# Kernel optimization log

Hardware: AMD Instinct MI355X
Metric: run time of the kernel (lower is better)

Reference implementation:

```python
import jax, jax.numpy as jnp
import numpy as np

N, E, G = 50000, 800000, 512
DIN, HID, DOUT, L, DE = 64, 64, 128, 3, 16
NEG_SLOPE = 0.2
BN_EPS = 1e-5


def setup_inputs() -> dict:
    key = jax.random.key(0)
    ks = jax.random.split(key, 20)
    s = 0.1  # weight scale for numerical stability
    return {
        "x": jax.random.normal(ks[0], (N, DIN), jnp.float32),
        "edge_index": jax.random.randint(ks[1], (2, E), 0, N, jnp.int32),
        "edge_attr": jax.random.normal(ks[2], (E, DE), jnp.float32),
        "batch": jnp.sort(jax.random.randint(ks[3], (N,), 0, G, jnp.int32)),
        "emb_W": jax.random.normal(ks[4], (HID, DIN), jnp.float32) * s,
        "emb_b": jax.random.normal(ks[5], (HID,), jnp.float32) * s,
        "Wl": jax.random.normal(ks[6], (L, HID, HID), jnp.float32) * s,
        "bl": jax.random.normal(ks[7], (L, HID), jnp.float32) * s,
        "Wr": jax.random.normal(ks[8], (L, HID, HID), jnp.float32) * s,
        "br": jax.random.normal(ks[9], (L, HID), jnp.float32) * s,
        "We": jax.random.normal(ks[10], (L, HID, DE), jnp.float32) * s,
        "att": jax.random.normal(ks[11], (L, HID), jnp.float32) * s,
        "conv_bias": jax.random.normal(ks[12], (L, HID), jnp.float32) * s,
        "bn_gamma": jax.random.uniform(ks[13], (L, HID), jnp.float32, 0.5, 1.5),
        "bn_beta": jax.random.normal(ks[14], (L, HID), jnp.float32) * s,
        "bn_mean": jnp.zeros((L, HID), jnp.float32),
        "bn_var": jnp.ones((L, HID), jnp.float32),
        "lin_W": jax.random.normal(ks[15], (DOUT, HID), jnp.float32) * s,
        "lin_b": jax.random.normal(ks[16], (DOUT,), jnp.float32) * s,
    }


def _gatv2(h, src, dst, edge_attr, Wl, bl, Wr, br, We, att, bias):
    # GATv2Conv, heads=1, concat=False, with edge features
    xl = h @ Wl.T + bl                      # [N,C] source transform (also message value)
    xr = h @ Wr.T + br                      # [N,C] target transform
    ea = edge_attr @ We.T                   # [E,C]
    m = xl[src] + xr[dst] + ea              # [E,C]
    m = jax.nn.leaky_relu(m, NEG_SLOPE)
    alpha = m @ att                         # [E] attention logits
    amax = jax.ops.segment_max(alpha, dst, num_segments=N)
    ea_exp = jnp.exp(alpha - amax[dst])
    denom = jax.ops.segment_sum(ea_exp, dst, num_segments=N)
    alpha = ea_exp / (denom[dst] + 1e-16)
    out = jax.ops.segment_sum(alpha[:, None] * xl[src], dst, num_segments=N)
    return out + bias


def reference(x, edge_index, edge_attr, batch, emb_W, emb_b, Wl, bl, Wr, br,
              We, att, conv_bias, bn_gamma, bn_beta, bn_mean, bn_var, lin_W, lin_b):
    src, dst = edge_index[0], edge_index[1]
    h = x @ emb_W.T + emb_b
    for i in range(L):
        hc = _gatv2(h, src, dst, edge_attr, Wl[i], bl[i], Wr[i], br[i],
                    We[i], att[i], conv_bias[i])
        # BatchNorm (eval mode, running stats)
        hc = (hc - bn_mean[i]) * jax.lax.rsqrt(bn_var[i] + BN_EPS) * bn_gamma[i] + bn_beta[i]
        hc = jax.nn.gelu(hc, approximate=False)  # torch F.gelu default is exact erf
        h = h + hc                                # residual; dropout p=0 / eval -> identity
    out = h @ lin_W.T + lin_b                     # [N,DOUT]
    counts = jax.ops.segment_sum(jnp.ones((N,), out.dtype), batch, num_segments=G)
    pooled = jax.ops.segment_sum(out, batch, num_segments=G)
    return pooled / jnp.maximum(counts, 1.0)[:, None]
```

## Files before the change

kernel.cpp:

```cpp
#include <hip/hip_runtime.h>
#include <math.h>

#define NEG_SLOPE 0.2f
#define BN_EPS 1e-5f

template <int N> struct IC { static constexpr int v = N; };
template <bool B> struct BC { static constexpr bool v = B; };

typedef _Float16 half2v __attribute__((ext_vector_type(2)));
typedef _Float16 f16x8 __attribute__((ext_vector_type(8)));
typedef float f32x4v __attribute__((ext_vector_type(4)));

__device__ __forceinline__ half2v u2h(unsigned u) {
  union { unsigned u; half2v h; } c;
  c.u = u;
  return c.h;
}
__device__ __forceinline__ unsigned pkh(float lo, float hi) {
  union { half2v h; unsigned u; } c;
  c.h[0] = (_Float16)lo;
  c.h[1] = (_Float16)hi;
  return c.u;
}

#if defined(__has_builtin)
#if __has_builtin(__builtin_amdgcn_fdot2)
#define FDOT2(a, b, c) __builtin_amdgcn_fdot2((a), (b), (c), false)
#endif
#endif
#ifndef FDOT2
__device__ __forceinline__ float fdot2_sw(half2v a, half2v b, float c) {
  return c + (float)a[0] * (float)b[0] + (float)a[1] * (float)b[1];
}
#define FDOT2(a, b, c) fdot2_sw((a), (b), (c))
#endif

#if defined(__has_builtin)
#if __has_builtin(__builtin_amdgcn_exp2f)
#define FEXP(x) __builtin_amdgcn_exp2f(x)
#define ATT_SCALE 1.44269504088896f
#endif
#endif
#ifndef FEXP
#define FEXP(x) __expf(x)
#define ATT_SCALE 1.0f
#endif

#define FMA4(acc, v, wq) \
  acc += (v).x * (wq).x + (v).y * (wq).y + (v).z * (wq).z + (v).w * (wq).w

#define DOT_ROW(buf, stride, r, bias, OUT)                                  \
  {                                                                         \
    __builtin_amdgcn_sched_barrier(0);                                      \
    float a0 = 0.f, a1 = 0.f, a2 = 0.f, a3 = 0.f;                           \
    _Pragma("unroll") for (int q = 0; q < 4; q++) {                         \
      float4 v0 = *(const float4*)((buf) + (r) * (stride) + q * 16 + 0);    \
      float4 v1 = *(const float4*)((buf) + (r) * (stride) + q * 16 + 4);    \
      float4 v2 = *(const float4*)((buf) + (r) * (stride) + q * 16 + 8);    \
      float4 v3 = *(const float4*)((buf) + (r) * (stride) + q * 16 + 12);   \
      FMA4(a0, v0, W[q * 4 + 0]);                                           \
      FMA4(a1, v1, W[q * 4 + 1]);                                           \
      FMA4(a2, v2, W[q * 4 + 2]);                                           \
      FMA4(a3, v3, W[q * 4 + 3]);                                           \
    }                                                                       \
    OUT = (bias) + ((a0 + a1) + (a2 + a3));                                 \
  }

__device__ __forceinline__ float wave_sum64(float v) {
  int x;
  x = __builtin_amdgcn_update_dpp(0, __float_as_int(v), 0x121, 0xF, 0xF, true);
  v += __int_as_float(x);
  x = __builtin_amdgcn_update_dpp(0, __float_as_int(v), 0x122, 0xF, 0xF, true);
  v += __int_as_float(x);
  x = __builtin_amdgcn_update_dpp(0, __float_as_int(v), 0x124, 0xF, 0xF, true);
  v += __int_as_float(x);
  x = __builtin_amdgcn_update_dpp(0, __float_as_int(v), 0x128, 0xF, 0xF, true);
  v += __int_as_float(x);
  x = __builtin_amdgcn_update_dpp(0, __float_as_int(v), 0x142, 0xF, 0xF, true);
  v += __int_as_float(x);
  x = __builtin_amdgcn_update_dpp(0, __float_as_int(v), 0x143, 0xF, 0xF, true);
  v += __int_as_float(x);
  return __int_as_float(__builtin_amdgcn_readlane(__float_as_int(v), 63));
}

#if defined(__has_builtin)
#if __has_builtin(__builtin_amdgcn_mfma_f32_16x16x32_f16)
#define HAVE_MFMA16 1
#endif
#endif

__global__ __launch_bounds__(256) void hist_kernel(
    const int* __restrict__ dst, const int* __restrict__ batch,
    int* __restrict__ deg, float* __restrict__ counts,
    const float* __restrict__ Wl, const float* __restrict__ Wr,
    _Float16* __restrict__ w16, int E_, int N_) {
  int i = blockIdx.x * 256 + threadIdx.x;
  if (i < E_) atomicAdd(&deg[dst[i]], 1);
  if (i < N_) atomicAdd(&counts[batch[i]], 1.0f);
  if (i < 24576)
    w16[i] = (i < 12288) ? (_Float16)Wl[i] : (_Float16)Wr[i - 12288];
}

__global__ __launch_bounds__(256) void scanA_kernel(
    const int* __restrict__ deg, int* __restrict__ row_ptr,
    int* __restrict__ segTot, int* __restrict__ bins, int N_, int nseg) {
  __shared__ int sb[256];
  __shared__ int lb[128];
  int t = threadIdx.x;
  if (t < 128) lb[t] = 0;
  __syncthreads();
  for (int s = blockIdx.x; s < nseg; s += gridDim.x) {
    int i = s * 256 + t;
    int v = (i < N_) ? deg[i] : 0;
    if (i < N_) atomicAdd(&lb[127 - min(v, 127)], 1);
    sb[t] = v;
    __syncthreads();
    for (int off = 1; off < 256; off <<= 1) {
      int a = (t >= off) ? sb[t - off] : 0;
      __syncthreads();
      sb[t] += a;
      __syncthreads();
    }
    int incl = sb[t];
    if (i < N_) row_ptr[i] = incl - v;
    if (t == 255) segTot[s] = incl;
    __syncthreads();
  }
  if (t < 128 && lb[t]) atomicAdd(&bins[t], lb[t]);
}

__global__ __launch_bounds__(256) void scanB_kernel(int* __restrict__ segTot,
                                                    int* __restrict__ bins,
                                                    int nseg) {
  __shared__ int sb[256];
  __shared__ int baseSh;
  int t = threadIdx.x;
  if (t == 0) baseSh = 0;
  __syncthreads();
  for (int c0 = 0; c0 < nseg; c0 += 256) {
    int s = c0 + t;
    int v = (s < nseg) ? segTot[s] : 0;
    sb[t] = v;
    __syncthreads();
    for (int off = 1; off < 256; off <<= 1) {
      int a = (t >= off) ? sb[t - off] : 0;
      __syncthreads();
      sb[t] += a;
      __syncthreads();
    }
    int incl = sb[t];
    int base = baseSh;
    if (s < nseg) segTot[s] = base + incl - v;
    __syncthreads();
    if (t == 255) baseSh = base + incl;
    __syncthreads();
  }
  int v2 = (t < 128) ? bins[t] : 0;
  sb[t] = v2;
  __syncthreads();
  for (int off = 1; off < 256; off <<= 1) {
    int a = (t >= off) ? sb[t - off] : 0;
    __syncthreads();
    sb[t] += a;
    __syncthreads();
  }
  if (t < 128) bins[t] = sb[t] - v2;
}

__global__ __launch_bounds__(256) void scanC_kernel(
    int* __restrict__ row_ptr, const int* __restrict__ segTot,
    int* __restrict__ cursor, const int* __restrict__ deg,
    int* __restrict__ bins, int* __restrict__ perm,
    int* __restrict__ csr_src, int* __restrict__ csr_eid, int N_, int E_) {
  __shared__ int lb[128];
  __shared__ int lbase[128];
  int t = threadIdx.x;
  if (t < 128) lb[t] = 0;
  __syncthreads();
  int i = blockIdx.x * 256 + t;
  int bin = 0, rk = 0;
  bool ok = (i < N_);
  if (ok) {
    int rp = row_ptr[i] + segTot[i >> 8];
    row_ptr[i] = rp;
    cursor[i] = rp;
    int dg = deg[i];
    bin = 127 - min(dg, 127);
    rk = atomicAdd(&lb[bin], 1);
  }
  if (i == 0) row_ptr[N_] = E_;
  if (blockIdx.x == 0 && t < 16) {
    csr_src[E_ + t] = 0;
    csr_eid[E_ + t] = 0;
  }
  __syncthreads();
  if (t < 128) {
    int c = lb[t];
    lbase[t] = c ? atomicAdd(&bins[t], c) : 0;
  }
  __syncthreads();
  if (ok) perm[lbase[bin] + rk] = i;
}

__global__ __launch_bounds__(256) void scatter_kernel(
    const int* __restrict__ src, const int* __restrict__ dst,
    int* __restrict__ cursor, int* __restrict__ csr_src,
    int* __restrict__ csr_eid, int E_) {
  int e = blockIdx.x * 256 + threadIdx.x;
  if (e >= E_) return;
  int pos = atomicAdd(&cursor[dst[e]], 1);
  csr_src[pos] = src[e];
  csr_eid[pos] = e;
}

__global__ __launch_bounds__(256) void permute_attr_kernel(
    const float4* __restrict__ edge_attr4, const int* __restrict__ csr_eid,
    unsigned* __restrict__ attr_u, int E_) {
  int p = blockIdx.x * 256 + threadIdx.x;
  if (p >= E_) return;
  int e = csr_eid[p];
  float4 a0 = edge_attr4[(size_t)e * 4 + 0];
  float4 a1 = edge_attr4[(size_t)e * 4 + 1];
  float4 a2 = edge_attr4[(size_t)e * 4 + 2];
  float4 a3 = edge_attr4[(size_t)e * 4 + 3];
  uint4 u0, u1;
  u0.x = pkh(a0.x, a0.y);
  u0.y = pkh(a0.z, a0.w);
  u0.z = pkh(a1.x, a1.y);
  u0.w = pkh(a1.z, a1.w);
  u1.x = pkh(a2.x, a2.y);
  u1.y = pkh(a2.z, a2.w);
  u1.z = pkh(a3.x, a3.y);
  u1.w = pkh(a3.z, a3.w);
  uint4* d4 = (uint4*)(attr_u + (size_t)p * 8);
  d4[0] = u0;
  d4[1] = u1;
}

__global__ __launch_bounds__(256, 3) void emb_kernel(
    const float* __restrict__ x, const float* __restrict__ emb_W,
    const float* __restrict__ emb_b, const _Float16* __restrict__ Wl16,
    const float* __restrict__ bl, const _Float16* __restrict__ Wr16,
    const float* __restrict__ br, float* __restrict__ h,
    _Float16* __restrict__ xl, _Float16* __restrict__ xr, int rows) {
  __shared__ float sx[4096];
  __shared__ float sh[64 * 68];
  int lane = threadIdx.x & 63;
  int w = threadIdx.x >> 6;
  int n0 = blockIdx.x * 64;

  {
    int gmax = rows * 64 - 4;
#pragma unroll
    for (int i = 0; i < 4; i++) {
      int off = w * 1024 + i * 256 + lane * 4;
      int g = min(n0 * 64 + off, gmax);
      *(float4*)(sx + off) = *(const float4*)(x + g);
    }
  }

  {
    float4 W[16];
#pragma unroll
    for (int q = 0; q < 16; q++) W[q] = ((const float4*)(emb_W + lane * 64))[q];
    float b = emb_b[lane];
#pragma unroll 1
    for (int t = 0; t < 16; t++) {
      int r = w * 16 + t;
      float a;
      DOT_ROW(sx, 64, r, b, a);
      sh[r * 68 + lane] = a;
      int n = n0 + r;
      if (n < rows) h[(size_t)n * 64 + lane] = a;
    }
  }

#ifdef HAVE_MFMA16
  {
    int r = lane & 15;
    int kg = lane >> 4;
    int nb = n0 + w * 16;
    const float* p = sh + (w * 16 + r) * 68 + kg * 8;
    f16x8 A0, A1;
    {
      float4 xa = *(const float4*)(p);
      float4 xb = *(const float4*)(p + 4);
      A0[0] = (_Float16)xa.x; A0[1] = (_Float16)xa.y;
      A0[2] = (_Float16)xa.z; A0[3] = (_Float16)xa.w;
      A0[4] = (_Float16)xb.x; A0[5] = (_Float16)xb.y;
      A0[6] = (_Float16)xb.z; A0[7] = (_Float16)xb.w;
      xa = *(const float4*)(p + 32);
      xb = *(const float4*)(p + 36);
      A1[0] = (_Float16)xa.x; A1[1] = (_Float16)xa.y;
      A1[2] = (_Float16)xa.z; A1[3] = (_Float16)xa.w;
      A1[4] = (_Float16)xb.x; A1[5] = (_Float16)xb.y;
      A1[6] = (_Float16)xb.z; A1[7] = (_Float16)xb.w;
    }
#pragma unroll
    for (int c = 0; c < 4; c++) {
      int o = c * 16 + r;
      {
        const f16x8* b0 = (const f16x8*)(Wl16 + (size_t)o * 64 + kg * 8);
        const f16x8* b1 = (const f16x8*)(Wl16 + (size_t)o * 64 + 32 + kg * 8);
        f32x4v acc;
        float bv = bl[o];
        acc[0] = bv; acc[1] = bv; acc[2] = bv; acc[3] = bv;
        acc = __builtin_amdgcn_mfma_f32_16x16x32_f16(A0, b0[0], acc, 0, 0, 0);
        acc = __builtin_amdgcn_mfma_f32_16x16x32_f16(A1, b1[0], acc, 0, 0, 0);
#pragma unroll
        for (int g = 0; g < 4; g++) {
          int nd = nb + kg * 4 + g;
          if (nd < rows) xl[(size_t)nd * 64 + o] = (_Float16)acc[g];
        }
      }
      {
        const f16x8* b0 = (const f16x8*)(Wr16 + (size_t)o * 64 + kg * 8);
        const f16x8* b1 = (const f16x8*)(Wr16 + (size_t)o * 64 + 32 + kg * 8);
        f32x4v acc;
        float bv = br[o];
        acc[0] = bv; acc[1] = bv; acc[2] = bv; acc[3] = bv;
        acc = __builtin_amdgcn_mfma_f32_16x16x32_f16(A0, b0[0], acc, 0, 0, 0);
        acc = __builtin_amdgcn_mfma_f32_16x16x32_f16(A1, b1[0], acc, 0, 0, 0);
#pragma unroll
        for (int g = 0; g < 4; g++) {
          int nd = nb + kg * 4 + g;
          if (nd < rows) xr[(size_t)nd * 64 + o] = (_Float16)acc[g];
        }
      }
    }
  }
#endif
}

__global__ __launch_bounds__(256) void linx_mfma_kernel(
    const float* __restrict__ in, const _Float16* __restrict__ Wl16,
    const float* __restrict__ bl, const _Float16* __restrict__ Wr16,
    const float* __restrict__ br, _Float16* __restrict__ xl,
    _Float16* __restrict__ xr, int rows) {
#ifdef HAVE_MFMA16
  int lane = threadIdx.x & 63;
  int w = threadIdx.x >> 6;
  int n0 = blockIdx.x * 64 + w * 16;
  int r = lane & 15;
  int kg = lane >> 4;

  int nA = min(n0 + r, rows - 1);
  f16x8 A0, A1;
  {
    const float* p = in + (size_t)nA * 64 + kg * 8;
    float4 xa = *(const float4*)(p);
    float4 xb = *(const float4*)(p + 4);
    A0[0] = (_Float16)xa.x; A0[1] = (_Float16)xa.y;
    A0[2] = (_Float16)xa.z; A0[3] = (_Float16)xa.w;
    A0[4] = (_Float16)xb.x; A0[5] = (_Float16)xb.y;
    A0[6] = (_Float16)xb.z; A0[7] = (_Float16)xb.w;
    xa = *(const float4*)(p + 32);
    xb = *(const float4*)(p + 36);
    A1[0] = (_Float16)xa.x; A1[1] = (_Float16)xa.y;
    A1[2] = (_Float16)xa.z; A1[3] = (_Float16)xa.w;
    A1[4] = (_Float16)xb.x; A1[5] = (_Float16)xb.y;
    A1[6] = (_Float16)xb.z; A1[7] = (_Float16)xb.w;
  }

#pragma unroll
  for (int c = 0; c < 4; c++) {
    int o = c * 16 + r;
    {
      const f16x8* b0 = (const f16x8*)(Wl16 + (size_t)o * 64 + kg * 8);
      const f16x8* b1 = (const f16x8*)(Wl16 + (size_t)o * 64 + 32 + kg * 8);
      f32x4v acc;
      float bv = bl[o];
      acc[0] = bv; acc[1] = bv; acc[2] = bv; acc[3] = bv;
      acc = __builtin_amdgcn_mfma_f32_16x16x32_f16(A0, b0[0], acc, 0, 0, 0);
      acc = __builtin_amdgcn_mfma_f32_16x16x32_f16(A1, b1[0], acc, 0, 0, 0);
#pragma unroll
      for (int g = 0; g < 4; g++) {
        int nd = n0 + kg * 4 + g;
        if (nd < rows) xl[(size_t)nd * 64 + o] = (_Float16)acc[g];
      }
    }
    {
      const f16x8* b0 = (const f16x8*)(Wr16 + (size_t)o * 64 + kg * 8);
      const f16x8* b1 = (const f16x8*)(Wr16 + (size_t)o * 64 + 32 + kg * 8);
      f32x4v acc;
      float bv = br[o];
      acc[0] = bv; acc[1] = bv; acc[2] = bv; acc[3] = bv;
      acc = __builtin_amdgcn_mfma_f32_16x16x32_f16(A0, b0[0], acc, 0, 0, 0);
      acc = __builtin_amdgcn_mfma_f32_16x16x32_f16(A1, b1[0], acc, 0, 0, 0);
#pragma unroll
      for (int g = 0; g < 4; g++) {
        int nd = n0 + kg * 4 + g;
        if (nd < rows) xr[(size_t)nd * 64 + o] = (_Float16)acc[g];
      }
    }
  }
#endif
}

template <bool CONTIG>
__global__ __launch_bounds__(256) void gat_fused_kernel(
    const int* __restrict__ perm, const int* __restrict__ csr_src,
    const int* __restrict__ csr_eid, const int* __restrict__ row_ptr,
    const unsigned* __restrict__ attr_u, const float* __restrict__ edge_attr,
    const _Float16* __restrict__ xl, const _Float16* __restrict__ xr,
    const float* __restrict__ We, const float* __restrict__ att,
    const float* __restrict__ conv_bias, const float* __restrict__ gamma,
    const float* __restrict__ beta, const float* __restrict__ mean,
    const float* __restrict__ var, float* __restrict__ h, int N_) {
  int widx = (blockIdx.x * 256 + threadIdx.x) >> 6;
  if (widx >= N_) return;
  int d = __builtin_amdgcn_readfirstlane(perm[widx]);
  int j = threadIdx.x & 63;
  half2v Wek2[8];
  float Wekf[16];
  if constexpr (CONTIG) {
#pragma unroll
    for (int q = 0; q < 8; q++) {
      Wek2[q][0] = (_Float16)We[j * 16 + 2 * q];
      Wek2[q][1] = (_Float16)We[j * 16 + 2 * q + 1];
    }
  } else {
#pragma unroll
    for (int k = 0; k < 16; k++) Wekf[k] = We[j * 16 + k];
  }
  float att_j = att[j] * ATT_SCALE;
  float sc = rsqrtf(var[j] + BN_EPS) * gamma[j];
  float sh = (conv_bias[j] - mean[j]) * sc + beta[j];

  int beg = __builtin_amdgcn_readfirstlane(row_ptr[d]);
  int end = __builtin_amdgcn_readfirstlane(row_ptr[d + 1]);
  float xrj = (float)xr[(size_t)d * 64 + j];
  float m = -INFINITY, l = 0.f, acc = 0.f;

  auto chunk = [&](int base, auto C_, auto PAD_) {
    constexpr int C = decltype(C_)::v;
    constexpr bool PAD = decltype(PAD_)::v;
    int si[C];
#pragma unroll
    for (int t = 0; t < C; t++) {
      int idx = PAD ? min(base + t, end - 1) : (base + t);
      si[t] = __builtin_amdgcn_readfirstlane(csr_src[idx]);
    }
    float xlv[C];
#pragma unroll
    for (int t = 0; t < C; t++)
      xlv[t] = (float)xl[(size_t)si[t] * 64 + j];
    float v[C];
#pragma unroll
    for (int t = 0; t < C; t++) {
      int idx = PAD ? min(base + t, end - 1) : (base + t);
      float ea;
      if constexpr (CONTIG) {
        const uint4* ap = (const uint4*)(attr_u + (size_t)idx * 8);
        uint4 ua = ap[0], ub = ap[1];
        ea = 0.f;
        ea = FDOT2(u2h(ua.x), Wek2[0], ea);
        ea = FDOT2(u2h(ua.y), Wek2[1], ea);
        ea = FDOT2(u2h(ua.z), Wek2[2], ea);
        ea = FDOT2(u2h(ua.w), Wek2[3], ea);
        ea = FDOT2(u2h(ub.x), Wek2[4], ea);
        ea = FDOT2(u2h(ub.y), Wek2[5], ea);
        ea = FDOT2(u2h(ub.z), Wek2[6], ea);
        ea = FDOT2(u2h(ub.w), Wek2[7], ea);
      } else {
        const float4* ap =
            (const float4*)(edge_attr + (size_t)csr_eid[idx] * 16);
        float4 a0 = ap[0], a1 = ap[1], a2 = ap[2], a3 = ap[3];
        ea = a0.x * Wekf[0]  + a0.y * Wekf[1]  + a0.z * Wekf[2]  + a0.w * Wekf[3]
           + a1.x * Wekf[4]  + a1.y * Wekf[5]  + a1.z * Wekf[6]  + a1.w * Wekf[7]
           + a2.x * Wekf[8]  + a2.y * Wekf[9]  + a2.z * Wekf[10] + a2.w * Wekf[11]
           + a3.x * Wekf[12] + a3.y * Wekf[13] + a3.z * Wekf[14] + a3.w * Wekf[15];
      }
      float z = xlv[t] + xrj + ea;
      z = fmaxf(z, NEG_SLOPE * z);
      float p = wave_sum64(z * att_j);
      v[t] = (!PAD || (base + t < end)) ? p : -INFINITY;
    }
    float mc = v[0];
#pragma unroll
    for (int t = 1; t < C; t++) mc = fmaxf(mc, v[t]);
    float newm = fmaxf(m, mc);
    float s = FEXP(m - newm);
    l *= s;
    acc *= s;
#pragma unroll
    for (int t = 0; t < C; t++) {
      float w = FEXP(v[t] - newm);
      l += w;
      acc += w * xlv[t];
    }
    m = newm;
  };

  int base = beg;
  for (; base + 16 <= end; base += 16) chunk(base, IC<16>{}, BC<false>{});
  if (base + 8 <= end) {
    chunk(base, IC<8>{}, BC<false>{});
    base += 8;
  }
  if (base + 4 <= end) {
    chunk(base, IC<4>{}, BC<false>{});
    base += 4;
  }
  if (base < end) chunk(base, IC<4>{}, BC<true>{});

  float val = acc / (l + 1e-16f) * sc + sh;
  float g = 0.5f * val * (1.f + erff(val * 0.70710678118654752f));
  h[(size_t)d * 64 + j] += g;
}

__global__ __launch_bounds__(256, 2) void lin_pool_kernel(
    const float* __restrict__ h, const float* __restrict__ lin_W,
    const float* __restrict__ lin_b, const int* __restrict__ batch,
    const float* __restrict__ counts, float* __restrict__ pooled, int rows) {
  __shared__ float shh[4096];
  int lane = threadIdx.x & 63;
  int w = threadIdx.x >> 6;
  int n0 = blockIdx.x * 64;

  {
    int gmax = rows * 64 - 4;
#pragma unroll
    for (int i = 0; i < 4; i++) {
      int off = w * 1024 + i * 256 + lane * 4;
      int g = min(n0 * 64 + off, gmax);
      *(float4*)(shh + off) = *(const float4*)(h + g);
    }
  }

  float4 W0[16], W1[16];
#pragma unroll
  for (int q = 0; q < 16; q++) W0[q] = ((const float4*)(lin_W + lane * 64))[q];
#pragma unroll
  for (int q = 0; q < 16; q++)
    W1[q] = ((const float4*)(lin_W + (lane + 64) * 64))[q];
  float b0 = lin_b[lane], b1 = lin_b[lane + 64];

  int curg = -1;
  float acc0 = 0.f, acc1 = 0.f;
  int lim = min(16, rows - n0 - w * 16);
#pragma unroll 1
  for (int t = 0; t < lim; t++) {
    int r = w * 16 + t;
    __builtin_amdgcn_sched_barrier(0);
    float d0 = b0, d1 = b1;
#pragma unroll
    for (int q = 0; q < 16; q++) {
      float4 v = *(const float4*)(shh + r * 64 + q * 4);
      FMA4(d0, v, W0[q]);
      FMA4(d1, v, W1[q]);
    }
    int g = batch[n0 + r];
    if (g != curg) {
      if (curg >= 0) {
        float inv = 1.f / fmaxf(counts[curg], 1.f);
        atomicAdd(&pooled[curg * 128 + lane], acc0 * inv);
        atomicAdd(&pooled[curg * 128 + 64 + lane], acc1 * inv);
      }
      curg = g;
      acc0 = 0.f;
      acc1 = 0.f;
    }
    acc0 += d0;
    acc1 += d1;
  }
  if (curg >= 0) {
    float inv = 1.f / fmaxf(counts[curg], 1.f);
    atomicAdd(&pooled[curg * 128 + lane], acc0 * inv);
    atomicAdd(&pooled[curg * 128 + 64 + lane], acc1 * inv);
  }
}

extern "C" void kernel_launch(void* const* d_in, const int* in_sizes, int n_in,
                              void* d_out, int out_size, void* d_ws, size_t ws_size,
                              hipStream_t stream) {
  const float* x         = (const float*)d_in[0];
  const int*   edge_index= (const int*)  d_in[1];
  const float* edge_attr = (const float*)d_in[2];
  const int*   batch     = (const int*)  d_in[3];
  const float* emb_W     = (const float*)d_in[4];
  const float* emb_b     = (const float*)d_in[5];
  const float* Wl        = (const float*)d_in[6];
  const float* bl        = (const float*)d_in[7];
  const float* Wr        = (const float*)d_in[8];
  const float* br        = (const float*)d_in[9];
  const float* We        = (const float*)d_in[10];
  const float* att       = (const float*)d_in[11];
  const float* conv_bias = (const float*)d_in[12];
  const float* bn_gamma  = (const float*)d_in[13];
  const float* bn_beta   = (const float*)d_in[14];
  const float* bn_mean   = (const float*)d_in[15];
  const float* bn_var    = (const float*)d_in[16];
  const float* lin_W     = (const float*)d_in[17];
  const float* lin_b     = (const float*)d_in[18];

  const int N_ = in_sizes[0] / 64;
  const int E_ = in_sizes[1] / 2;
  const int G_ = out_size / 128;
  const int* src = edge_index;
  const int* dst = edge_index + E_;

  const int Npad = (N_ + 3) & ~3;
  const int Epad = (E_ + 19) & ~3;
  const int nseg = (N_ + 255) / 256;

  float* ws      = (float*)d_ws;
  float* h       = ws;
  _Float16* xl   = (_Float16*)(h + (size_t)N_ * 64);
  _Float16* xr   = xl + (size_t)N_ * 64;
  int*   csr_src = (int*)(xr + (size_t)N_ * 64);
  int*   csr_eid = csr_src + Epad;
  int*   row_ptr = csr_eid + Epad;
  int*   cursor  = row_ptr + (Npad + 4);
  int*   deg     = cursor + Npad;
  float* counts  = (float*)(deg + Npad);
  int*   segTot  = (int*)(counts + G_);
  int*   bins    = segTot + nseg + 8;
  int*   perm    = bins + 128;
  uintptr_t abp  = (uintptr_t)(perm + Npad);
  abp = (abp + 15) & ~(uintptr_t)15;
  _Float16* w16  = (_Float16*)abp;
  uintptr_t abp2 = abp + 24576 * sizeof(_Float16);
  unsigned* attr_u = (unsigned*)abp2;

  size_t base_bytes = (abp2 - (uintptr_t)d_ws);
  bool contig = ws_size >= base_bytes + (size_t)E_ * 32 + 64;

  const int hgrid = (max(E_, N_) + 255) / 256;
  const int ngrid = (N_ + 255) / 256;
  const int egrid = (E_ + 255) / 256;

  hipMemsetAsync(deg, 0, ((size_t)Npad + G_ + nseg + 8 + 128) * 4, stream);
  hist_kernel<<<hgrid, 256, 0, stream>>>(dst, batch, deg, counts, Wl, Wr,
                                         w16, E_, N_);
  scanA_kernel<<<min(nseg, 1024), 256, 0, stream>>>(deg, row_ptr, segTot,
                                                    bins, N_, nseg);
  scanB_kernel<<<1, 256, 0, stream>>>(segTot, bins, nseg);
  scanC_kernel<<<ngrid, 256, 0, stream>>>(row_ptr, segTot, cursor, deg, bins,
                                          perm, csr_src, csr_eid, N_, E_);
  scatter_kernel<<<egrid, 256, 0, stream>>>(src, dst, cursor, csr_src,
                                            csr_eid, E_);
  if (contig) {
    permute_attr_kernel<<<egrid, 256, 0, stream>>>(
        (const float4*)edge_attr, csr_eid, attr_u, E_);
  }

  const int tgrid = (N_ + 63) / 64;
  emb_kernel<<<tgrid, 256, 0, stream>>>(x, emb_W, emb_b, w16, bl,
                                        w16 + 12288, br, h, xl, xr, N_);

  const int gatBlocks = (N_ + 3) / 4;
  for (int l = 0; l < 3; l++) {
    if (l > 0) {
      linx_mfma_kernel<<<tgrid, 256, 0, stream>>>(
          h, w16 + (size_t)l * 4096, bl + l * 64,
          w16 + 12288 + (size_t)l * 4096, br + l * 64, xl, xr, N_);
    }
    if (contig) {
      gat_fused_kernel<true><<<gatBlocks, 256, 0, stream>>>(
          perm, csr_src, csr_eid, row_ptr, attr_u, edge_attr, xl, xr,
          We + (size_t)l * 1024, att + l * 64, conv_bias + l * 64,
          bn_gamma + l * 64, bn_beta + l * 64, bn_mean + l * 64,
          bn_var + l * 64, h, N_);
    } else {
      gat_fused_kernel<false><<<gatBlocks, 256, 0, stream>>>(
          perm, csr_src, csr_eid, row_ptr, attr_u, edge_attr, xl, xr,
          We + (size_t)l * 1024, att + l * 64, conv_bias + l * 64,
          bn_gamma + l * 64, bn_beta + l * 64, bn_mean + l * 64,
          bn_var + l * 64, h, N_);
    }
  }

  hipMemsetAsync(d_out, 0, (size_t)G_ * 128 * 4, stream);
  lin_pool_kernel<<<(N_ + 63) / 64, 256, 0, stream>>>(
      h, lin_W, lin_b, batch, counts, (float*)d_out, N_);
}
```

Baseline: 544.8 us.

## Process four edges per wave in GAT kernel with 16 lanes per edge

Result: slower. 628.6 us (+15.4%).

```diff
diff --git a/kernel.cpp b/kernel.cpp
--- a/kernel.cpp
+++ b/kernel.cpp
@@ -5,7 +5,6 @@
 #define BN_EPS 1e-5f
 
 template <int N> struct IC { static constexpr int v = N; };
-template <bool B> struct BC { static constexpr bool v = B; };
 
 typedef _Float16 half2v __attribute__((ext_vector_type(2)));
 typedef _Float16 f16x8 __attribute__((ext_vector_type(8)));
@@ -66,7 +65,7 @@
     OUT = (bias) + ((a0 + a1) + (a2 + a3));                                 \
   }
 
-__device__ __forceinline__ float wave_sum64(float v) {
+__device__ __forceinline__ float row_sum16(float v) {
   int x;
   x = __builtin_amdgcn_update_dpp(0, __float_as_int(v), 0x121, 0xF, 0xF, true);
   v += __int_as_float(x);
@@ -76,11 +75,7 @@
   v += __int_as_float(x);
   x = __builtin_amdgcn_update_dpp(0, __float_as_int(v), 0x128, 0xF, 0xF, true);
   v += __int_as_float(x);
-  x = __builtin_amdgcn_update_dpp(0, __float_as_int(v), 0x142, 0xF, 0xF, true);
-  v += __int_as_float(x);
-  x = __builtin_amdgcn_update_dpp(0, __float_as_int(v), 0x143, 0xF, 0xF, true);
-  v += __int_as_float(x);
-  return __int_as_float(__builtin_amdgcn_readlane(__float_as_int(v), 63));
+  return v;
 }
 
 #if defined(__has_builtin)
@@ -93,12 +88,18 @@
     const int* __restrict__ dst, const int* __restrict__ batch,
     int* __restrict__ deg, float* __restrict__ counts,
     const float* __restrict__ Wl, const float* __restrict__ Wr,
-    _Float16* __restrict__ w16, int E_, int N_) {
+    const float* __restrict__ We, _Float16* __restrict__ w16, int E_,
+    int N_) {
   int i = blockIdx.x * 256 + threadIdx.x;
   if (i < E_) atomicAdd(&deg[dst[i]], 1);
   if (i < N_) atomicAdd(&counts[batch[i]], 1.0f);
-  if (i < 24576)
-    w16[i] = (i < 12288) ? (_Float16)Wl[i] : (_Float16)Wr[i - 12288];
+  if (i < 12288) {
+    w16[i] = (_Float16)Wl[i];
+  } else if (i < 24576) {
+    w16[i] = (_Float16)Wr[i - 12288];
+  } else if (i < 27648) {
+    w16[i] = (_Float16)We[i - 24576];
+  }
 }
 
 __global__ __launch_bounds__(256) void scanA_kernel(
@@ -403,110 +404,214 @@
     const int* __restrict__ csr_eid, const int* __restrict__ row_ptr,
     const unsigned* __restrict__ attr_u, const float* __restrict__ edge_attr,
     const _Float16* __restrict__ xl, const _Float16* __restrict__ xr,
-    const float* __restrict__ We, const float* __restrict__ att,
-    const float* __restrict__ conv_bias, const float* __restrict__ gamma,
-    const float* __restrict__ beta, const float* __restrict__ mean,
-    const float* __restrict__ var, float* __restrict__ h, int N_) {
+    const _Float16* __restrict__ we16, const float* __restrict__ We,
+    const float* __restrict__ att, const float* __restrict__ conv_bias,
+    const float* __restrict__ gamma, const float* __restrict__ beta,
+    const float* __restrict__ mean, const float* __restrict__ var,
+    float* __restrict__ h, int N_) {
   int widx = (blockIdx.x * 256 + threadIdx.x) >> 6;
   if (widx >= N_) return;
   int d = __builtin_amdgcn_readfirstlane(perm[widx]);
-  int j = threadIdx.x & 63;
-  half2v Wek2[8];
-  float Wekf[16];
+  int lane = threadIdx.x & 63;
+  int jj = lane & 15;
+  int eg = lane >> 4;
+
+  half2v Wk[4][8];
+  float Wf[4][16];
   if constexpr (CONTIG) {
-#pragma unroll
-    for (int q = 0; q < 8; q++) {
-      Wek2[q][0] = (_Float16)We[j * 16 + 2 * q];
-      Wek2[q][1] = (_Float16)We[j * 16 + 2 * q + 1];
+    const uint4* wp = (const uint4*)(we16 + jj * 64);
+#pragma unroll
+    for (int i = 0; i < 4; i++) {
+      uint4 wa = wp[2 * i], wb = wp[2 * i + 1];
+      Wk[i][0] = u2h(wa.x);
+      Wk[i][1] = u2h(wa.y);
+      Wk[i][2] = u2h(wa.z);
+      Wk[i][3] = u2h(wa.w);
+      Wk[i][4] = u2h(wb.x);
+      Wk[i][5] = u2h(wb.y);
+      Wk[i][6] = u2h(wb.z);
+      Wk[i][7] = u2h(wb.w);
     }
   } else {
 #pragma unroll
-    for (int k = 0; k < 16; k++) Wekf[k] = We[j * 16 + k];
-  }
-  float att_j = att[j] * ATT_SCALE;
-  float sc = rsqrtf(var[j] + BN_EPS) * gamma[j];
-  float sh = (conv_bias[j] - mean[j]) * sc + beta[j];
+    for (int i = 0; i < 4; i++)
+#pragma unroll
+      for (int k = 0; k < 16; k++) Wf[i][k] = We[(4 * jj + i) * 16 + k];
+  }
+  float4 attv = *(const float4*)(att + jj * 4);
+  float at0 = attv.x * ATT_SCALE, at1 = attv.y * ATT_SCALE;
+  float at2 = attv.z * ATT_SCALE, at3 = attv.w * ATT_SCALE;
+  float4 varv = *(const float4*)(var + jj * 4);
+  float4 gamv = *(const float4*)(gamma + jj * 4);
+  float4 cbv = *(const float4*)(conv_bias + jj * 4);
+  float4 mev = *(const float4*)(mean + jj * 4);
+  float4 bev = *(const float4*)(beta + jj * 4);
+  float sc0 = rsqrtf(varv.x + BN_EPS) * gamv.x;
+  float sh0 = (cbv.x - mev.x) * sc0 + bev.x;
+  float sc1 = rsqrtf(varv.y + BN_EPS) * gamv.y;
+  float sh1 = (cbv.y - mev.y) * sc1 + bev.y;
+  float sc2 = rsqrtf(varv.z + BN_EPS) * gamv.z;
+  float sh2 = (cbv.z - mev.z) * sc2 + bev.z;
+  float sc3 = rsqrtf(varv.w + BN_EPS) * gamv.w;
+  float sh3 = (cbv.w - mev.w) * sc3 + bev.w;
 
   int beg = __builtin_amdgcn_readfirstlane(row_ptr[d]);
   int end = __builtin_amdgcn_readfirstlane(row_ptr[d + 1]);
-  float xrj = (float)xr[(size_t)d * 64 + j];
-  float m = -INFINITY, l = 0.f, acc = 0.f;
-
-  auto chunk = [&](int base, auto C_, auto PAD_) {
+  int deg = end - beg;
+  int degm1 = max(deg - 1, 0);
+
+  float xr0, xr1, xr2, xr3;
+  {
+    uint2 xp = *(const uint2*)((const char*)xr + (size_t)d * 128 + jj * 8);
+    half2v h0 = u2h(xp.x), h1 = u2h(xp.y);
+    xr0 = (float)h0[0];
+    xr1 = (float)h0[1];
+    xr2 = (float)h1[0];
+    xr3 = (float)h1[1];
+  }
+
+  float m = -INFINITY, l = 0.f;
+  float a0 = 0.f, a1 = 0.f, a2 = 0.f, a3 = 0.f;
+
+  auto chunk = [&](int base, auto C_) {
     constexpr int C = decltype(C_)::v;
-    constexpr bool PAD = decltype(PAD_)::v;
+    int idxv[C];
+    bool msk[C];
+#pragma unroll
+    for (int k = 0; k < C; k++) {
+      int t = base + k * 4 + eg;
+      idxv[k] = beg + min(t, degm1);
+      msk[k] = t < deg;
+    }
     int si[C];
 #pragma unroll
-    for (int t = 0; t < C; t++) {
-      int idx = PAD ? min(base + t, end - 1) : (base + t);
-      si[t] = __builtin_amdgcn_readfirstlane(csr_src[idx]);
-    }
-    float xlv[C];
-#pragma unroll
-    for (int t = 0; t < C; t++)
-      xlv[t] = (float)xl[(size_t)si[t] * 64 + j];
+    for (int k = 0; k < C; k++) si[k] = csr_src[idxv[k]];
+    uint2 xpk[C];
+#pragma unroll
+    for (int k = 0; k < C; k++)
+      xpk[k] = *(const uint2*)((const char*)xl + (size_t)si[k] * 128 + jj * 8);
     float v[C];
 #pragma unroll
-    for (int t = 0; t < C; t++) {
-      int idx = PAD ? min(base + t, end - 1) : (base + t);
-      float ea;
+    for (int k = 0; k < C; k++) {
+      float ea0, ea1, ea2, ea3;
       if constexpr (CONTIG) {
-        const uint4* ap = (const uint4*)(attr_u + (size_t)idx * 8);
+        const uint4* ap = (const uint4*)(attr_u + (size_t)idxv[k] * 8);
         uint4 ua = ap[0], ub = ap[1];
-        ea = 0.f;
-        ea = FDOT2(u2h(ua.x), Wek2[0], ea);
-        ea = FDOT2(u2h(ua.y), Wek2[1], ea);
-        ea = FDOT2(u2h(ua.z), Wek2[2], ea);
-        ea = FDOT2(u2h(ua.w), Wek2[3], ea);
-        ea = FDOT2(u2h(ub.x), Wek2[4], ea);
-        ea = FDOT2(u2h(ub.y), Wek2[5], ea);
-        ea = FDOT2(u2h(ub.z), Wek2[6], ea);
-        ea = FDOT2(u2h(ub.w), Wek2[7], ea);
+        ea0 = 0.f; ea1 = 0.f; ea2 = 0.f; ea3 = 0.f;
+        half2v c0 = u2h(ua.x), c1 = u2h(ua.y), c2 = u2h(ua.z), c3 = u2h(ua.w);
+        half2v c4 = u2h(ub.x), c5 = u2h(ub.y), c6 = u2h(ub.z), c7 = u2h(ub.w);
+        ea0 = FDOT2(c0, Wk[0][0], ea0); ea0 = FDOT2(c1, Wk[0][1], ea0);
+        ea0 = FDOT2(c2, Wk[0][2], ea0); ea0 = FDOT2(c3, Wk[0][3], ea0);
+        ea0 = FDOT2(c4, Wk[0][4], ea0); ea0 = FDOT2(c5, Wk[0][5], ea0);
+        ea0 = FDOT2(c6, Wk[0][6], ea0); ea0 = FDOT2(c7, Wk[0][7], ea0);
+        ea1 = FDOT2(c0, Wk[1][0], ea1); ea1 = FDOT2(c1, Wk[1][1], ea1);
+        ea1 = FDOT2(c2, Wk[1][2], ea1); ea1 = FDOT2(c3, Wk[1][3], ea1);
+        ea1 = FDOT2(c4, Wk[1][4], ea1); ea1 = FDOT2(c5, Wk[1][5], ea1);
+        ea1 = FDOT2(c6, Wk[1][6], ea1); ea1 = FDOT2(c7, Wk[1][7], ea1);
+        ea2 = FDOT2(c0, Wk[2][0], ea2); ea2 = FDOT2(c1, Wk[2][1], ea2);
+        ea2 = FDOT2(c2, Wk[2][2], ea2); ea2 = FDOT2(c3, Wk[2][3], ea2);
+        ea2 = FDOT2(c4, Wk[2][4], ea2); ea2 = FDOT2(c5, Wk[2][5], ea2);
+        ea2 = FDOT2(c6, Wk[2][6], ea2); ea2 = FDOT2(c7, Wk[2][7], ea2);
+        ea3 = FDOT2(c0, Wk[3][0], ea3); ea3 = FDOT2(c1, Wk[3][1], ea3);
+        ea3 = FDOT2(c2, Wk[3][2], ea3); ea3 = FDOT2(c3, Wk[3][3], ea3);
+        ea3 = FDOT2(c4, Wk[3][4], ea3); ea3 = FDOT2(c5, Wk[3][5], ea3);
+        ea3 = FDOT2(c6, Wk[3][6], ea3); ea3 = FDOT2(c7, Wk[3][7], ea3);
       } else {
-        const float4* ap =
-            (const float4*)(edge_attr + (size_t)csr_eid[idx] * 16);
-        float4 a0 = ap[0], a1 = ap[1], a2 = ap[2], a3 = ap[3];
-        ea = a0.x * Wekf[0]  + a0.y * Wekf[1]  + a0.z * Wekf[2]  + a0.w * Wekf[3]
-           + a1.x * Wekf[4]  + a1.y * Wekf[5]  + a1.z * Wekf[6]  + a1.w * Wekf[7]
-           + a2.x * Wekf[8]  + a2.y * Wekf[9]  + a2.z * Wekf[10] + a2.w * Wekf[11]
-           + a3.x * Wekf[12] + a3.y * Wekf[13] + a3.z * Wekf[14] + a3.w * Wekf[15];
+        int e = csr_eid[idxv[k]];
+        const float4* ap = (const float4*)(edge_attr + (size_t)e * 16);
+        float4 q0 = ap[0], q1 = ap[1], q2 = ap[2], q3 = ap[3];
+        ea0 = q0.x * Wf[0][0] + q0.y * Wf[0][1] + q0.z * Wf[0][2] + q0.w * Wf[0][3]
+            + q1.x * Wf[0][4] + q1.y * Wf[0][5] + q1.z * Wf[0][6] + q1.w * Wf[0][7]
+            + q2.x * Wf[0][8] + q2.y * Wf[0][9] + q2.z * Wf[0][10] + q2.w * Wf[0][11]
+            + q3.x * Wf[0][12] + q3.y * Wf[0][13] + q3.z * Wf[0][14] + q3.w * Wf[0][15];
+        ea1 = q0.x * Wf[1][0] + q0.y * Wf[1][1] + q0.z * Wf[1][2] + q0.w * Wf[1][3]
+            + q1.x * Wf[1][4] + q1.y * Wf[1][5] + q1.z * Wf[1][6] + q1.w * Wf[1][7]
+            + q2.x * Wf[1][8] + q2.y * Wf[1][9] + q2.z * Wf[1][10] + q2.w * Wf[1][11]
+            + q3.x * Wf[1][12] + q3.y * Wf[1][13] + q3.z * Wf[1][14] + q3.w * Wf[1][15];
+        ea2 = q0.x * Wf[2][0] + q0.y * Wf[2][1] + q0.z * Wf[2][2] + q0.w * Wf[2][3]
+            + q1.x * Wf[2][4] + q1.y * Wf[2][5] + q1.z * Wf[2][6] + q1.w * Wf[2][7]
+            + q2.x * Wf[2][8] + q2.y * Wf[2][9] + q2.z * Wf[2][10] + q2.w * Wf[2][11]
+            + q3.x * Wf[2][12] + q3.y * Wf[2][13] + q3.z * Wf[2][14] + q3.w * Wf[2][15];
+        ea3 = q0.x * Wf[3][0] + q0.y * Wf[3][1] + q0.z * Wf[3][2] + q0.w * Wf[3][3]
+            + q1.x * Wf[3][4] + q1.y * Wf[3][5] + q1.z * Wf[3][6] + q1.w * Wf[3][7]
+            + q2.x * Wf[3][8] + q2.y * Wf[3][9] + q2.z * Wf[3][10] + q2.w * Wf[3][11]
+            + q3.x * Wf[3][12] + q3.y * Wf[3][13] + q3.z * Wf[3][14] + q3.w * Wf[3][15];
       }
-      float z = xlv[t] + xrj + ea;
-      z = fmaxf(z, NEG_SLOPE * z);
-      float p = wave_sum64(z * att_j);
-      v[t] = (!PAD || (base + t < end)) ? p : -INFINITY;
+      half2v h0 = u2h(xpk[k].x), h1 = u2h(xpk[k].y);
+      float z0 = (float)h0[0] + xr0 + ea0;
+      z0 = fmaxf(z0, NEG_SLOPE * z0);
+      float z1 = (float)h0[1] + xr1 + ea1;
+      z1 = fmaxf(z1, NEG_SLOPE * z1);
+      float z2 = (float)h1[0] + xr2 + ea2;
+      z2 = fmaxf(z2, NEG_SLOPE * z2);
+      float z3 = (float)h1[1] + xr3 + ea3;
+      z3 = fmaxf(z3, NEG_SLOPE * z3);
+      float p = (z0 * at0 + z1 * at1) + (z2 * at2 + z3 * at3);
+      p = row_sum16(p);
+      v[k] = msk[k] ? p : -INFINITY;
     }
     float mc = v[0];
 #pragma unroll
-    for (int t = 1; t < C; t++) mc = fmaxf(mc, v[t]);
+    for (int k = 1; k < C; k++) mc = fmaxf(mc, v[k]);
+    mc = fmaxf(mc, __shfl_xor(mc, 16, 64));
+    mc = fmaxf(mc, __shfl_xor(mc, 32, 64));
     float newm = fmaxf(m, mc);
     float s = FEXP(m - newm);
     l *= s;
-    acc *= s;
-#pragma unroll
-    for (int t = 0; t < C; t++) {
-      float w = FEXP(v[t] - newm);
+    a0 *= s;
+    a1 *= s;
+    a2 *= s;
+    a3 *= s;
+#pragma unroll
+    for (int k = 0; k < C; k++) {
+      float w = FEXP(v[k] - newm);
       l += w;
-      acc += w * xlv[t];
+      half2v h0 = u2h(xpk[k].x), h1 = u2h(xpk[k].y);
+      a0 += w * (float)h0[0];
+      a1 += w * (float)h0[1];
+      a2 += w * (float)h1[0];
+      a3 += w * (float)h1[1];
     }
     m = newm;
   };
 
-  int base = beg;
-  for (; base + 16 <= end; base += 16) chunk(base, IC<16>{}, BC<false>{});
-  if (base + 8 <= end) {
-    chunk(base, IC<8>{}, BC<false>{});
+  int base = 0;
+  for (; base + 16 <= deg; base += 16) chunk(base, IC<4>{});
+  if (base + 8 <= deg) {
+    chunk(base, IC<2>{});
     base += 8;
   }
-  if (base + 4 <= end) {
-    chunk(base, IC<4>{}, BC<false>{});
-    base += 4;
-  }
-  if (base < end) chunk(base, IC<4>{}, BC<true>{});
-
-  float val = acc / (l + 1e-16f) * sc + sh;
-  float g = 0.5f * val * (1.f + erff(val * 0.70710678118654752f));
-  h[(size_t)d * 64 + j] += g;
+  if (base < deg) chunk(base, IC<2>{});
+
+  l += __shfl_xor(l, 16, 64);
+  l += __shfl_xor(l, 32, 64);
+  a0 += __shfl_xor(a0, 16, 64);
+  a0 += __shfl_xor(a0, 32, 64);
+  a1 += __shfl_xor(a1, 16, 64);
+  a1 += __shfl_xor(a1, 32, 64);
+  a2 += __shfl_xor(a2, 16, 64);
+  a2 += __shfl_xor(a2, 32, 64);
+  a3 += __shfl_xor(a3, 16, 64);
+  a3 += __shfl_xor(a3, 32, 64);
+
+  if (eg == 0) {
+    float den = l + 1e-16f;
+    float v0 = a0 / den * sc0 + sh0;
+    float v1 = a1 / den * sc1 + sh1;
+    float v2 = a2 / den * sc2 + sh2;
+    float v3 = a3 / den * sc3 + sh3;
+    float g0 = 0.5f * v0 * (1.f + erff(v0 * 0.70710678118654752f));
+    float g1 = 0.5f * v1 * (1.f + erff(v1 * 0.70710678118654752f));
+    float g2 = 0.5f * v2 * (1.f + erff(v2 * 0.70710678118654752f));
+    float g3 = 0.5f * v3 * (1.f + erff(v3 * 0.70710678118654752f));
+    float4* hp = (float4*)(h + (size_t)d * 64 + jj * 4);
+    float4 o = *hp;
+    o.x += g0;
+    o.y += g1;
+    o.z += g2;
+    o.w += g3;
+    *hp = o;
+  }
 }
 
 __global__ __launch_bounds__(256, 2) void lin_pool_kernel(
@@ -620,7 +725,8 @@
   uintptr_t abp  = (uintptr_t)(perm + Npad);
   abp = (abp + 15) & ~(uintptr_t)15;
   _Float16* w16  = (_Float16*)abp;
-  uintptr_t abp2 = abp + 24576 * sizeof(_Float16);
+  uintptr_t abp2 = abp + 27648 * sizeof(_Float16);
+  abp2 = (abp2 + 15) & ~(uintptr_t)15;
   unsigned* attr_u = (unsigned*)abp2;
 
   size_t base_bytes = (abp2 - (uintptr_t)d_ws);
@@ -631,7 +737,7 @@
   const int egrid = (E_ + 255) / 256;
 
   hipMemsetAsync(deg, 0, ((size_t)Npad + G_ + nseg + 8 + 128) * 4, stream);
-  hist_kernel<<<hgrid, 256, 0, stream>>>(dst, batch, deg, counts, Wl, Wr,
+  hist_kernel<<<hgrid, 256, 0, stream>>>(dst, batch, deg, counts, Wl, Wr, We,
                                          w16, E_, N_);
   scanA_kernel<<<min(nseg, 1024), 256, 0, stream>>>(deg, row_ptr, segTot,
                                                     bins, N_, nseg);
@@ -656,15 +762,16 @@
           h, w16 + (size_t)l * 4096, bl + l * 64,
           w16 + 12288 + (size_t)l * 4096, br + l * 64, xl, xr, N_);
     }
+    const _Float16* we16 = w16 + 24576 + (size_t)l * 1024;
     if (contig) {
       gat_fused_kernel<true><<<gatBlocks, 256, 0, stream>>>(
-          perm, csr_src, csr_eid, row_ptr, attr_u, edge_attr, xl, xr,
+          perm, csr_src, csr_eid, row_ptr, attr_u, edge_attr, xl, xr, we16,
           We + (size_t)l * 1024, att + l * 64, conv_bias + l * 64,
           bn_gamma + l * 64, bn_beta + l * 64, bn_mean + l * 64,
           bn_var + l * 64, h, N_);
     } else {
       gat_fused_kernel<false><<<gatBlocks, 256, 0, stream>>>(
-          perm, csr_src, csr_eid, row_ptr, attr_u, edge_attr, xl, xr,
+          perm, csr_src, csr_eid, row_ptr, attr_u, edge_attr, xl, xr, we16,
           We + (size_t)l * 1024, att + l * 64, conv_bias + l * 64,
           bn_gamma + l * 64, bn_beta + l * 64, bn_mean + l * 64,
           bn_var + l * 64, h, N_);
```

## Record edge ranks during histogram, drop scatter atomics; binary-search graph counts

Applied to the files above, without the earlier changes.

New measurement: 513.5 us. 1.06x faster.

```diff
diff --git a/kernel.cpp b/kernel.cpp
--- a/kernel.cpp
+++ b/kernel.cpp
@@ -89,14 +89,12 @@
 #endif
 #endif
 
-__global__ __launch_bounds__(256) void hist_kernel(
-    const int* __restrict__ dst, const int* __restrict__ batch,
-    int* __restrict__ deg, float* __restrict__ counts,
-    const float* __restrict__ Wl, const float* __restrict__ Wr,
-    _Float16* __restrict__ w16, int E_, int N_) {
+__global__ __launch_bounds__(256) void edge_pass1_kernel(
+    const int* __restrict__ dst, int* __restrict__ deg,
+    int* __restrict__ tmp_pos, const float* __restrict__ Wl,
+    const float* __restrict__ Wr, _Float16* __restrict__ w16, int E_) {
   int i = blockIdx.x * 256 + threadIdx.x;
-  if (i < E_) atomicAdd(&deg[dst[i]], 1);
-  if (i < N_) atomicAdd(&counts[batch[i]], 1.0f);
+  if (i < E_) tmp_pos[i] = atomicAdd(&deg[dst[i]], 1);
   if (i < 24576)
     w16[i] = (i < 12288) ? (_Float16)Wl[i] : (_Float16)Wr[i - 12288];
 }
@@ -129,9 +127,10 @@
   if (t < 128 && lb[t]) atomicAdd(&bins[t], lb[t]);
 }
 
-__global__ __launch_bounds__(256) void scanB_kernel(int* __restrict__ segTot,
-                                                    int* __restrict__ bins,
-                                                    int nseg) {
+__global__ __launch_bounds__(256) void scanB_kernel(
+    int* __restrict__ segTot, int* __restrict__ bins,
+    const int* __restrict__ batch, float* __restrict__ counts, int nseg,
+    int N_, int G_) {
   __shared__ int sb[256];
   __shared__ int baseSh;
   int t = threadIdx.x;
@@ -165,13 +164,27 @@
     __syncthreads();
   }
   if (t < 128) bins[t] = sb[t] - v2;
+  for (int g = t; g < G_; g += 256) {
+    int lo = 0, hi = N_;
+    while (lo < hi) {
+      int mid = (lo + hi) >> 1;
+      if (batch[mid] < g) lo = mid + 1; else hi = mid;
+    }
+    int lb0 = lo;
+    hi = N_;
+    while (lo < hi) {
+      int mid = (lo + hi) >> 1;
+      if (batch[mid] < g + 1) lo = mid + 1; else hi = mid;
+    }
+    counts[g] = (float)(lo - lb0);
+  }
 }
 
 __global__ __launch_bounds__(256) void scanC_kernel(
     int* __restrict__ row_ptr, const int* __restrict__ segTot,
-    int* __restrict__ cursor, const int* __restrict__ deg,
-    int* __restrict__ bins, int* __restrict__ perm,
-    int* __restrict__ csr_src, int* __restrict__ csr_eid, int N_, int E_) {
+    const int* __restrict__ deg, int* __restrict__ bins,
+    int* __restrict__ perm, int* __restrict__ csr_src,
+    int* __restrict__ csr_eid, int N_, int E_) {
   __shared__ int lb[128];
   __shared__ int lbase[128];
   int t = threadIdx.x;
@@ -183,7 +196,6 @@
   if (ok) {
     int rp = row_ptr[i] + segTot[i >> 8];
     row_ptr[i] = rp;
-    cursor[i] = rp;
     int dg = deg[i];
     bin = 127 - min(dg, 127);
     rk = atomicAdd(&lb[bin], 1);
@@ -202,13 +214,13 @@
   if (ok) perm[lbase[bin] + rk] = i;
 }
 
-__global__ __launch_bounds__(256) void scatter_kernel(
+__global__ __launch_bounds__(256) void edge_pass2_kernel(
     const int* __restrict__ src, const int* __restrict__ dst,
-    int* __restrict__ cursor, int* __restrict__ csr_src,
-    int* __restrict__ csr_eid, int E_) {
+    const int* __restrict__ row_ptr, const int* __restrict__ tmp_pos,
+    int* __restrict__ csr_src, int* __restrict__ csr_eid, int E_) {
   int e = blockIdx.x * 256 + threadIdx.x;
   if (e >= E_) return;
-  int pos = atomicAdd(&cursor[dst[e]], 1);
+  int pos = row_ptr[dst[e]] + tmp_pos[e];
   csr_src[pos] = src[e];
   csr_eid[pos] = e;
 }
@@ -611,8 +623,8 @@
   int*   csr_src = (int*)(xr + (size_t)N_ * 64);
   int*   csr_eid = csr_src + Epad;
   int*   row_ptr = csr_eid + Epad;
-  int*   cursor  = row_ptr + (Npad + 4);
-  int*   deg     = cursor + Npad;
+  int*   tmp_pos = row_ptr + (Npad + 4);
+  int*   deg     = tmp_pos + Epad;
   float* counts  = (float*)(deg + Npad);
   int*   segTot  = (int*)(counts + G_);
   int*   bins    = segTot + nseg + 8;
@@ -626,20 +638,20 @@
   size_t base_bytes = (abp2 - (uintptr_t)d_ws);
   bool contig = ws_size >= base_bytes + (size_t)E_ * 32 + 64;
 
-  const int hgrid = (max(E_, N_) + 255) / 256;
   const int ngrid = (N_ + 255) / 256;
   const int egrid = (E_ + 255) / 256;
 
   hipMemsetAsync(deg, 0, ((size_t)Npad + G_ + nseg + 8 + 128) * 4, stream);
-  hist_kernel<<<hgrid, 256, 0, stream>>>(dst, batch, deg, counts, Wl, Wr,
-                                         w16, E_, N_);
+  edge_pass1_kernel<<<egrid, 256, 0, stream>>>(dst, deg, tmp_pos, Wl, Wr,
+                                               w16, E_);
   scanA_kernel<<<min(nseg, 1024), 256, 0, stream>>>(deg, row_ptr, segTot,
                                                     bins, N_, nseg);
-  scanB_kernel<<<1, 256, 0, stream>>>(segTot, bins, nseg);
-  scanC_kernel<<<ngrid, 256, 0, stream>>>(row_ptr, segTot, cursor, deg, bins,
-                                          perm, csr_src, csr_eid, N_, E_);
-  scatter_kernel<<<egrid, 256, 0, stream>>>(src, dst, cursor, csr_src,
-                                            csr_eid, E_);
+  scanB_kernel<<<1, 256, 0, stream>>>(segTot, bins, batch, counts, nseg, N_,
+                                      G_);
+  scanC_kernel<<<ngrid, 256, 0, stream>>>(row_ptr, segTot, deg, bins, perm,
+                                          csr_src, csr_eid, N_, E_);
+  edge_pass2_kernel<<<egrid, 256, 0, stream>>>(src, dst, row_ptr, tmp_pos,
+                                               csr_src, csr_eid, E_);
   if (contig) {
     permute_attr_kernel<<<egrid, 256, 0, stream>>>(
         (const float4*)edge_attr, csr_eid, attr_u, E_);
```
